# Performance work log

Measured on AMD Instinct MI355X. Metric: run time of the kernel, lower is better.

Reference implementation:

```python
import jax, jax.numpy as jnp
import numpy as np

EPS = 1e-5
NEG_SLOPE = 0.2

def _bn(x, gamma, beta):
    # BatchNorm1d in training mode: stats over (batch, length) per channel. x: [B,C,N]
    m = jnp.mean(x, axis=(0, 2), keepdims=True)
    v = jnp.mean((x - m) ** 2, axis=(0, 2), keepdims=True)  # biased variance
    return (x - m) * jax.lax.rsqrt(v + EPS) * gamma[None, :, None] + beta[None, :, None]

def setup_inputs() -> dict:
    key = jax.random.key(0)
    ks = jax.random.split(key, 7)
    B, C, N, H = 32, 64, 2048, 128
    s = 1.0 / np.sqrt(C)
    return {
        "x": jax.random.normal(ks[0], (B, C, N), dtype=jnp.float32),
        "wq": jax.random.normal(ks[1], (C, C), dtype=jnp.float32) * s,
        "wk": jax.random.normal(ks[2], (C, C), dtype=jnp.float32) * s,
        "wv": jax.random.normal(ks[3], (C, C), dtype=jnp.float32) * s,
        "w_ff1": jax.random.normal(ks[4], (H, C), dtype=jnp.float32) * s,
        "w_ff2": jax.random.normal(ks[5], (C, H), dtype=jnp.float32) * (1.0 / np.sqrt(H)),
        "bn1_gamma": jnp.ones((C,), dtype=jnp.float32),
        "bn1_beta": jnp.zeros((C,), dtype=jnp.float32),
        "bn2_gamma": jnp.ones((C,), dtype=jnp.float32),
        "bn2_beta": jnp.zeros((C,), dtype=jnp.float32),
    }

def reference(x, wq, wk, wv, w_ff1, w_ff2, bn1_gamma, bn1_beta, bn2_gamma, bn2_beta):
    # x: [B, C, N]; 1x1 convs are per-point channel matmuls
    C = x.shape[1]
    q = jnp.einsum('oc,bcn->bno', wq, x)          # [B,N,C]
    k = jnp.einsum('oc,bcn->bon', wk, x)          # [B,C,N]
    v = jnp.einsum('oc,bcn->bno', wv, x)          # [B,N,C] (v^T)
    energy = jnp.einsum('bnc,bcm->bnm', q, k)     # [B,N,N]
    attention = jax.nn.softmax(energy / jnp.sqrt(jnp.float32(C)), axis=-1)
    x_r = jnp.einsum('bnm,bmc->bcn', attention, v)  # [B,C,N]
    h = _bn(x + x_r, bn1_gamma, bn1_beta)
    ff = jnp.einsum('hc,bcn->bhn', w_ff1, h)      # [B,H,N]
    ff = jnp.where(ff >= 0, ff, NEG_SLOPE * ff)   # LeakyReLU(0.2)
    ff = jnp.einsum('ch,bhn->bcn', w_ff2, ff)     # [B,C,N]
    return _bn(h + ff, bn2_gamma, bn2_beta)
```

## Files before the change

### kernel.cpp

```cpp
#include <hip/hip_runtime.h>

#define B_ 32
#define C_ 64
#define N_ 2048
#define H_ 128

typedef unsigned short u16;
typedef unsigned int u32;
typedef float f32x4 __attribute__((ext_vector_type(4)));
typedef __bf16 bf16x8 __attribute__((ext_vector_type(8)));
typedef __bf16 bf16x4 __attribute__((ext_vector_type(4)));
typedef unsigned short u16x4 __attribute__((ext_vector_type(4)));

#define MFMA(a, b, c) __builtin_amdgcn_mfma_f32_16x16x32_bf16(a, b, c, 0, 0, 0)
#define LOG2E 1.44269504088896f

__device__ __forceinline__ int swz(int row, int cb) { return row * 128 + (cb ^ ((row & 7) << 4)); }
__device__ __forceinline__ int swz256(int row, int cb) { return row * 256 + (cb ^ ((row & 7) << 4)); }

__device__ __forceinline__ bf16x8 cvt8(const float* p, float s) {
    f32x4 a = *(const f32x4*)p, b = *(const f32x4*)(p + 4);
    bf16x8 o;
    o[0] = (__bf16)(a[0] * s); o[1] = (__bf16)(a[1] * s);
    o[2] = (__bf16)(a[2] * s); o[3] = (__bf16)(a[3] * s);
    o[4] = (__bf16)(b[0] * s); o[5] = (__bf16)(b[1] * s);
    o[6] = (__bf16)(b[2] * s); o[7] = (__bf16)(b[3] * s);
    return o;
}

__global__ __launch_bounds__(256) void qkv_k(
    const float* __restrict__ x,
    const float* __restrict__ wq, const float* __restrict__ wk, const float* __restrict__ wv,
    const float* __restrict__ w1, const float* __restrict__ w2,
    u16* __restrict__ Qg, u16* __restrict__ Kg, u16* __restrict__ Vg,
    u16* __restrict__ w1b, u16* __restrict__ w2b)
{
    const int b = blockIdx.y, nt = blockIdx.x, t = threadIdx.x;
    const int lane = t & 63, wave = t >> 6, g = lane >> 4, r16 = lane & 15;
    __shared__ __align__(16) u16 xT[128 * 64];
    const int n0 = nt * 128;

    bf16x8 wqf[4][2], wkf[4][2], wvf[4][2];
#pragma unroll
    for (int jt = 0; jt < 4; ++jt)
#pragma unroll
        for (int kc = 0; kc < 2; ++kc) {
            const int ro = (r16 + 16 * jt) * 64 + 8 * g + 32 * kc;
            wqf[jt][kc] = cvt8(wq + ro, 0.125f * LOG2E);
            wkf[jt][kc] = cvt8(wk + ro, 1.0f);
            wvf[jt][kc] = cvt8(wv + ro, 1.0f);
        }

    {
        int c = t >> 5;
        const int nn = (t & 31) * 4;
#pragma unroll
        for (int pass = 0; pass < 8; ++pass, c += 8) {
            f32x4 v = *(const f32x4*)&x[(size_t)(b * 64 + c) * 2048 + n0 + nn];
#pragma unroll
            for (int j = 0; j < 4; ++j)
                xT[swz(nn + j, 2 * c) >> 1] = __builtin_bit_cast(u16, (__bf16)v[j]);
        }
    }
    if (b == 0 && nt == 0) {
        for (int i = t; i < H_ * C_; i += 256) w1b[i] = __builtin_bit_cast(u16, (__bf16)w1[i]);
        for (int i = t; i < C_ * H_; i += 256) w2b[i] = __builtin_bit_cast(u16, (__bf16)w2[i]);
    }
    __syncthreads();

#pragma unroll
    for (int p = 0; p < 2; ++p) {
        const int nt16 = wave * 2 + p;
        bf16x8 xa[2];
#pragma unroll
        for (int kc = 0; kc < 2; ++kc)
            xa[kc] = *(const bf16x8*)&xT[swz(nt16 * 16 + r16, 16 * g + 64 * kc) >> 1];
#pragma unroll
        for (int jt = 0; jt < 4; ++jt) {
            f32x4 aq = {0.f, 0.f, 0.f, 0.f}, ak = {0.f, 0.f, 0.f, 0.f};
            aq = MFMA(wqf[jt][0], xa[0], aq); aq = MFMA(wqf[jt][1], xa[1], aq);
            ak = MFMA(wkf[jt][0], xa[0], ak); ak = MFMA(wkf[jt][1], xa[1], ak);
            bf16x4 qk, kk;
#pragma unroll
            for (int r = 0; r < 4; ++r) { qk[r] = (__bf16)aq[r]; kk[r] = (__bf16)ak[r]; }
            const size_t ro = (size_t)(b * 2048 + n0 + nt16 * 16 + r16) * 64 + 16 * jt + 4 * g;
            *(bf16x4*)&Qg[ro] = qk;
            *(bf16x4*)&Kg[ro] = kk;
        }
#pragma unroll
        for (int it = 0; it < 4; ++it) {
            f32x4 av = {0.f, 0.f, 0.f, 0.f};
            av = MFMA(xa[0], wvf[it][0], av);
            av = MFMA(xa[1], wvf[it][1], av);
            bf16x4 vk;
#pragma unroll
            for (int r = 0; r < 4; ++r) vk[r] = (__bf16)av[r];
            *(bf16x4*)&Vg[(size_t)(b * 64 + 16 * it + r16) * 2048 + n0 + nt16 * 16 + 4 * g] = vk;
        }
    }
}

__global__ __launch_bounds__(256) void attn_k(
    const u16* __restrict__ Qg, const u16* __restrict__ Kg, const u16* __restrict__ Vg,
    const float* __restrict__ x, float* __restrict__ y,
    float* __restrict__ ps, float* __restrict__ pq)
{
    const int t = threadIdx.x;
    const int lane = t & 63, wave = t >> 6, g = lane >> 4, r16 = lane & 15;
    const int L = blockIdx.x;
    const int xcd = L & 7, slot = L >> 3;
    const int b = xcd * 4 + (slot >> 4);
    const int qt = slot & 15;

    __shared__ __align__(16) u16 Kt[2][64 * 64];
    __shared__ __align__(16) u16 Vt[2][64 * 64];
    __shared__ __align__(16) u16 Pl[4][2][16 * 64];

    const int n0 = qt * 128 + wave * 32;
    bf16x8 qf[2][2];
#pragma unroll
    for (int u = 0; u < 2; ++u) {
        const u16* qrow = Qg + (size_t)(b * 2048 + n0 + 16 * u + r16) * 64 + 8 * g;
        qf[u][0] = *(const bf16x8*)qrow;
        qf[u][1] = *(const bf16x8*)(qrow + 32);
    }
    f32x4 xr[2][4];
#pragma unroll
    for (int u = 0; u < 2; ++u)
#pragma unroll
        for (int ct = 0; ct < 4; ++ct)
#pragma unroll
            for (int r = 0; r < 4; ++r)
                xr[u][ct][r] = x[(size_t)(b * 64 + 16 * ct + 4 * g + r) * 2048 + n0 + 16 * u + r16];

    f32x4 acc[2][4];
    float m[2] = {-1e30f, -1e30f}, lp[2] = {0.f, 0.f};
#pragma unroll
    for (int u = 0; u < 2; ++u)
#pragma unroll
        for (int ct = 0; ct < 4; ++ct) acc[u][ct] = (f32x4){0.f, 0.f, 0.f, 0.f};

    const char* Kgb = (const char*)Kg + (size_t)b * 2048 * 128;
    const char* Vgb = (const char*)Vg + (size_t)b * 64 * 4096;
    const int srcxor = (((lane & 7) ^ (lane >> 3)) << 4);
    const int rowb = wave * 16 + (lane >> 3);

    auto stage = [&](int kv, int buf) {
#pragma unroll
        for (int j = 0; j < 2; ++j) {
            const char* gk = Kgb + (size_t)(kv + rowb + 8 * j) * 128 + srcxor;
            const char* gv = Vgb + (size_t)(rowb + 8 * j) * 4096 + kv * 2 + srcxor;
            char* lk = (char*)&Kt[buf][0] + (wave * 2 + j) * 1024;
            char* lv = (char*)&Vt[buf][0] + (wave * 2 + j) * 1024;
            __builtin_amdgcn_global_load_lds(
                (const __attribute__((address_space(1))) void*)gk,
                (__attribute__((address_space(3))) void*)lk, 16, 0, 0);
            __builtin_amdgcn_global_load_lds(
                (const __attribute__((address_space(1))) void*)gv,
                (__attribute__((address_space(3))) void*)lv, 16, 0, 0);
        }
    };

    stage(0, 0);

#pragma unroll 1
    for (int kvt = 0; kvt < 32; ++kvt) {
        __syncthreads();
        if (kvt < 31) stage((kvt + 1) * 64, (kvt + 1) & 1);
        const char* Kc = (const char*)&Kt[kvt & 1][0];
        const char* Vc = (const char*)&Vt[kvt & 1][0];

        bf16x8 kf[4][2];
#pragma unroll
        for (int it = 0; it < 4; ++it)
#pragma unroll
            for (int kc = 0; kc < 2; ++kc)
                kf[it][kc] = *(const bf16x8*)(Kc + swz(16 * it + r16, 16 * g + 64 * kc));
        f32x4 s[2][4];
#pragma unroll
        for (int it = 0; it < 4; ++it) {
            f32x4 a0 = {0.f, 0.f, 0.f, 0.f}, a1 = {0.f, 0.f, 0.f, 0.f};
            a0 = MFMA(kf[it][0], qf[0][0], a0); a0 = MFMA(kf[it][1], qf[0][1], a0);
            a1 = MFMA(kf[it][0], qf[1][0], a1); a1 = MFMA(kf[it][1], qf[1][1], a1);
            s[0][it] = a0; s[1][it] = a1;
        }
        bf16x8 vf[4][2];
#pragma unroll
        for (int ct = 0; ct < 4; ++ct)
#pragma unroll
            for (int kc = 0; kc < 2; ++kc)
                vf[ct][kc] = *(const bf16x8*)(Vc + swz(16 * ct + r16, 16 * g + 64 * kc));

#pragma unroll
        for (int u = 0; u < 2; ++u) {
            float pm = s[u][0][0];
#pragma unroll
            for (int it = 0; it < 4; ++it)
#pragma unroll
                for (int r = 0; r < 4; ++r) pm = fmaxf(pm, s[u][it][r]);
            pm = fmaxf(pm, __shfl_xor(pm, 16, 64));
            pm = fmaxf(pm, __shfl_xor(pm, 32, 64));
            if (!__all(pm <= m[u] + 8.f)) {
                const float mn = fmaxf(m[u], pm);
                const float al = exp2f(m[u] - mn);
                m[u] = mn;
                lp[u] *= al;
#pragma unroll
                for (int ct = 0; ct < 4; ++ct)
#pragma unroll
                    for (int r = 0; r < 4; ++r) acc[u][ct][r] *= al;
            }
            float ls = 0.f;
#pragma unroll
            for (int it = 0; it < 4; ++it) {
                bf16x4 pk;
#pragma unroll
                for (int r = 0; r < 4; ++r) {
                    const float pv = exp2f(s[u][it][r] - m[u]);
                    ls += pv;
                    pk[r] = (__bf16)pv;
                }
                *(bf16x4*)((char*)Pl[wave][u] + swz(r16, 32 * it + 8 * g)) = pk;
            }
            lp[u] += ls;
            const bf16x8 pf0 = *(const bf16x8*)((const char*)Pl[wave][u] + swz(r16, 16 * g));
            const bf16x8 pf1 = *(const bf16x8*)((const char*)Pl[wave][u] + swz(r16, 16 * g + 64));
#pragma unroll
            for (int ct = 0; ct < 4; ++ct) {
                acc[u][ct] = MFMA(vf[ct][0], pf0, acc[u][ct]);
                acc[u][ct] = MFMA(vf[ct][1], pf1, acc[u][ct]);
            }
        }
    }

    float sv[4][4], qv[4][4];
#pragma unroll
    for (int ct = 0; ct < 4; ++ct)
#pragma unroll
        for (int r = 0; r < 4; ++r) { sv[ct][r] = 0.f; qv[ct][r] = 0.f; }
#pragma unroll
    for (int u = 0; u < 2; ++u) {
        float l = lp[u];
        l += __shfl_xor(l, 16, 64);
        l += __shfl_xor(l, 32, 64);
        const float inv = 1.0f / l;
        const int n = n0 + 16 * u + r16;
#pragma unroll
        for (int ct = 0; ct < 4; ++ct) {
            f32x4 o;
#pragma unroll
            for (int r = 0; r < 4; ++r) {
                o[r] = acc[u][ct][r] * inv + xr[u][ct][r];
                sv[ct][r] += o[r];
                qv[ct][r] += o[r] * o[r];
            }
            *(f32x4*)&y[(size_t)(b * 2048 + n) * 64 + 16 * ct + 4 * g] = o;
        }
    }
#pragma unroll
    for (int d = 1; d <= 8; d <<= 1)
#pragma unroll
        for (int ct = 0; ct < 4; ++ct)
#pragma unroll
            for (int r = 0; r < 4; ++r) {
                sv[ct][r] += __shfl_xor(sv[ct][r], d, 64);
                qv[ct][r] += __shfl_xor(qv[ct][r], d, 64);
            }
    __syncthreads();
    float* sb = (float*)&Pl[0][0][0];
    if (r16 == 0) {
#pragma unroll
        for (int ct = 0; ct < 4; ++ct)
#pragma unroll
            for (int r = 0; r < 4; ++r) {
                const int c = 16 * ct + 4 * g + r;
                sb[wave * 64 + c] = sv[ct][r];
                sb[256 + wave * 64 + c] = qv[ct][r];
            }
    }
    __syncthreads();
    if (t < 64) {
        ps[L * 64 + t] = sb[t] + sb[64 + t] + sb[128 + t] + sb[192 + t];
        pq[L * 64 + t] = sb[256 + t] + sb[320 + t] + sb[384 + t] + sb[448 + t];
    }
}

__global__ __launch_bounds__(256) void finalize_k(
    const float* __restrict__ psum, const float* __restrict__ psq,
    const float* __restrict__ gamma, const float* __restrict__ beta,
    float* __restrict__ ss, int nblk)
{
    const int c = blockIdx.x, t = threadIdx.x;
    const int lane = t & 63, wave = t >> 6;
    float s = 0.f, q = 0.f;
    for (int bl = t; bl < nblk; bl += 256) {
        s += psum[bl * 64 + c];
        q += psq[bl * 64 + c];
    }
#pragma unroll
    for (int d = 1; d <= 32; d <<= 1) {
        s += __shfl_xor(s, d, 64);
        q += __shfl_xor(q, d, 64);
    }
    __shared__ float ls[4], lq[4];
    if (lane == 0) { ls[wave] = s; lq[wave] = q; }
    __syncthreads();
    if (t == 0) {
        s = ls[0] + ls[1] + ls[2] + ls[3];
        q = lq[0] + lq[1] + lq[2] + lq[3];
        const float mean = s * (1.0f / 65536.0f);
        const float var  = q * (1.0f / 65536.0f) - mean * mean;
        const float sc   = rsqrtf(var + 1e-5f) * gamma[c];
        ss[c] = sc;
        ss[64 + c] = beta[c] - mean * sc;
    }
}

__global__ __launch_bounds__(256) void ff_k(
    const float* __restrict__ y, const float* __restrict__ ss1,
    const u16* __restrict__ w1b, const u16* __restrict__ w2b,
    float* __restrict__ z, float* __restrict__ ps, float* __restrict__ pq)
{
    const int b = blockIdx.y, nt = blockIdx.x, t = threadIdx.x;
    const int lane = t & 63, wave = t >> 6, g = lane >> 4, r16 = lane & 15;
    const int L = blockIdx.y * gridDim.x + blockIdx.x;
    __shared__ __align__(16) u16 hT[64 * 64];
    __shared__ __align__(16) float hf[64 * 68];
    __shared__ __align__(16) u16 pb[4][16 * 128];
    __shared__ float sc1[64], sh1[64];
    if (t < 64) { sc1[t] = ss1[t]; sh1[t] = ss1[64 + t]; }
    __syncthreads();
    const int n0 = nt * 64;
    {
        const int i = t >> 2, c0 = (t & 3) * 16;
        u16 hb[16] __attribute__((aligned(16)));
#pragma unroll
        for (int q4 = 0; q4 < 4; ++q4) {
            const int c = c0 + 4 * q4;
            f32x4 v = *(const f32x4*)&y[(size_t)(b * 2048 + n0 + i) * 64 + c];
            f32x4 hv;
#pragma unroll
            for (int j = 0; j < 4; ++j) hv[j] = v[j] * sc1[c + j] + sh1[c + j];
            *(f32x4*)&hf[i * 68 + c] = hv;
#pragma unroll
            for (int j = 0; j < 4; ++j) hb[4 * q4 + j] = __builtin_bit_cast(u16, (__bf16)hv[j]);
        }
        *(uint4*)&hT[swz(i, 2 * c0) >> 1]      = *(const uint4*)&hb[0];
        *(uint4*)&hT[swz(i, 2 * c0 + 16) >> 1] = *(const uint4*)&hb[8];
    }
    __syncthreads();

    bf16x8 ha[2];
#pragma unroll
    for (int kc = 0; kc < 2; ++kc)
        ha[kc] = *(const bf16x8*)&hT[swz(wave * 16 + r16, 16 * g + 64 * kc) >> 1];
#pragma unroll
    for (int it = 0; it < 8; ++it) {
        f32x4 a = {0.f, 0.f, 0.f, 0.f};
#pragma unroll
        for (int kc = 0; kc < 2; ++kc) {
            bf16x8 w1f = *(const bf16x8*)&w1b[(r16 + 16 * it) * 64 + 8 * g + 32 * kc];
            a = MFMA(w1f, ha[kc], a);
        }
        u16x4 pk;
#pragma unroll
        for (int r = 0; r < 4; ++r) {
            const float rv = a[r] >= 0.f ? a[r] : 0.2f * a[r];
            pk[r] = __builtin_bit_cast(u16, (__bf16)rv);
        }
        *(u16x4*)&pb[wave][swz256(r16, 2 * (16 * it + 4 * g)) >> 1] = pk;
    }
    bf16x8 pa[4];
#pragma unroll
    for (int kc = 0; kc < 4; ++kc)
        pa[kc] = *(const bf16x8*)&pb[wave][swz256(r16, 16 * g + 64 * kc) >> 1];
    const int nl = wave * 16 + r16;
    float sv[4][4], qv[4][4];
#pragma unroll
    for (int jt = 0; jt < 4; ++jt) {
        f32x4 a = {0.f, 0.f, 0.f, 0.f};
#pragma unroll
        for (int kc = 0; kc < 4; ++kc) {
            bf16x8 w2f = *(const bf16x8*)&w2b[(r16 + 16 * jt) * 128 + 8 * g + 32 * kc];
            a = MFMA(w2f, pa[kc], a);
        }
        f32x4 h4 = *(const f32x4*)&hf[nl * 68 + 16 * jt + 4 * g];
#pragma unroll
        for (int r = 0; r < 4; ++r) {
            a[r] += h4[r];
            sv[jt][r] = a[r];
            qv[jt][r] = a[r] * a[r];
        }
        *(f32x4*)&z[(size_t)(b * 2048 + n0 + nl) * 64 + 16 * jt + 4 * g] = a;
    }
#pragma unroll
    for (int d = 1; d <= 8; d <<= 1)
#pragma unroll
        for (int jt = 0; jt < 4; ++jt)
#pragma unroll
            for (int r = 0; r < 4; ++r) {
                sv[jt][r] += __shfl_xor(sv[jt][r], d, 64);
                qv[jt][r] += __shfl_xor(qv[jt][r], d, 64);
            }
    __syncthreads();
    float* sb = (float*)&pb[0][0];
    if (r16 == 0) {
#pragma unroll
        for (int jt = 0; jt < 4; ++jt)
#pragma unroll
            for (int r = 0; r < 4; ++r) {
                const int c = 16 * jt + 4 * g + r;
                sb[wave * 64 + c] = sv[jt][r];
                sb[256 + wave * 64 + c] = qv[jt][r];
            }
    }
    __syncthreads();
    if (t < 64) {
        ps[L * 64 + t] = sb[t] + sb[64 + t] + sb[128 + t] + sb[192 + t];
        pq[L * 64 + t] = sb[256 + t] + sb[320 + t] + sb[384 + t] + sb[448 + t];
    }
}

__global__ __launch_bounds__(256) void bnout_k(
    const float* __restrict__ z, const float* __restrict__ ss2, float* __restrict__ out)
{
    const int b = blockIdx.y, nt = blockIdx.x, t = threadIdx.x;
    __shared__ float tile[64 * 65];
    __shared__ float sc2[64], sh2[64];
    if (t < 64) { sc2[t] = ss2[t]; sh2[t] = ss2[64 + t]; }
    __syncthreads();
    const int n0 = nt * 64;
    {
        const int i = t >> 2, c0 = (t & 3) * 16;
#pragma unroll
        for (int q4 = 0; q4 < 4; ++q4) {
            const int c = c0 + 4 * q4;
            f32x4 v = *(const f32x4*)&z[(size_t)(b * 2048 + n0 + i) * 64 + c];
#pragma unroll
            for (int j = 0; j < 4; ++j)
                tile[(i)*65 + c + j] = v[j] * sc2[c + j] + sh2[c + j];
        }
    }
    __syncthreads();
    {
        const int c = t >> 2, j0 = (t & 3) * 16;
#pragma unroll
        for (int q4 = 0; q4 < 4; ++q4) {
            f32x4 ov;
#pragma unroll
            for (int j = 0; j < 4; ++j)
                ov[j] = tile[(j0 + 4 * q4 + j) * 65 + c];
            *(f32x4*)&out[(size_t)(b * 64 + c) * 2048 + n0 + j0 + 4 * q4] = ov;
        }
    }
}

extern "C" void kernel_launch(void* const* d_in, const int* in_sizes, int n_in,
                              void* d_out, int out_size, void* d_ws, size_t ws_size,
                              hipStream_t stream)
{
    const float* x   = (const float*)d_in[0];
    const float* wq  = (const float*)d_in[1];
    const float* wk  = (const float*)d_in[2];
    const float* wv  = (const float*)d_in[3];
    const float* w1  = (const float*)d_in[4];
    const float* w2  = (const float*)d_in[5];
    const float* g1  = (const float*)d_in[6];
    const float* be1 = (const float*)d_in[7];
    const float* g2  = (const float*)d_in[8];
    const float* be2 = (const float*)d_in[9];
    float* out = (float*)d_out;

    char* w = (char*)d_ws;
    u16* Qg = (u16*)w;   w += (size_t)B_ * N_ * C_ * 2;
    u16* Kg = (u16*)w;   w += (size_t)B_ * N_ * C_ * 2;
    u16* Vg = (u16*)w;   w += (size_t)B_ * N_ * C_ * 2;
    float* y = (float*)w; w += (size_t)B_ * N_ * C_ * 4;
    float* z = (float*)w; w += (size_t)B_ * N_ * C_ * 4;
    u16* w1b = (u16*)w;  w += (size_t)H_ * C_ * 2;
    u16* w2b = (u16*)w;  w += (size_t)C_ * H_ * 2;
    float* ps1 = (float*)w; w += 1024 * 64 * 4;
    float* pq1 = (float*)w; w += 1024 * 64 * 4;
    float* ps2 = (float*)w; w += 1024 * 64 * 4;
    float* pq2 = (float*)w; w += 1024 * 64 * 4;
    float* ss1 = (float*)w; w += 128 * 4;
    float* ss2 = (float*)w; w += 128 * 4;

    const dim3 blk(256);
    hipLaunchKernelGGL(qkv_k,   dim3(16, 32), blk, 0, stream, x, wq, wk, wv, w1, w2, Qg, Kg, Vg, w1b, w2b);
    hipLaunchKernelGGL(attn_k,  dim3(512),    blk, 0, stream, Qg, Kg, Vg, x, y, ps1, pq1);
    hipLaunchKernelGGL(finalize_k, dim3(64),  blk, 0, stream, ps1, pq1, g1, be1, ss1, 512);
    hipLaunchKernelGGL(ff_k,    dim3(32, 32), blk, 0, stream, y, ss1, w1b, w2b, z, ps2, pq2);
    hipLaunchKernelGGL(finalize_k, dim3(64),  blk, 0, stream, ps2, pq2, g2, be2, ss2, 1024);
    hipLaunchKernelGGL(bnout_k, dim3(32, 32), blk, 0, stream, z, ss2, out);
}
```

Baseline: 152.9 us.

## Store intermediates y and z in bf16 and restructure attention loop with setprio

The fp32 intermediates y and z become bf16, halving the traffic written by attn_k and ff_k and read back by ff_k and bnout_k. The attention kernel now uses one flat LDS buffer with precomputed swizzled offsets and manual double-buffer unrolling. It adds s_setprio around the MFMA blocks and tree-structured max and sum reductions. The residual x is loaded at the epilogue instead of being held in registers across the loop. The change adds bf16 rounding error to the residual stream before each BatchNorm.

```diff
diff --git a/kernel.cpp b/kernel.cpp
--- a/kernel.cpp
+++ b/kernel.cpp
@@ -17,6 +17,10 @@
 
 __device__ __forceinline__ int swz(int row, int cb) { return row * 128 + (cb ^ ((row & 7) << 4)); }
 __device__ __forceinline__ int swz256(int row, int cb) { return row * 256 + (cb ^ ((row & 7) << 4)); }
+
+__device__ __forceinline__ float b2f(u16 v) {
+    union { u32 u; float f; } x; x.u = ((u32)v) << 16; return x.f;
+}
 
 __device__ __forceinline__ bf16x8 cvt8(const float* p, float s) {
     f32x4 a = *(const f32x4*)p, b = *(const f32x4*)(p + 4);
@@ -102,7 +106,7 @@
 
 __global__ __launch_bounds__(256) void attn_k(
     const u16* __restrict__ Qg, const u16* __restrict__ Kg, const u16* __restrict__ Vg,
-    const float* __restrict__ x, float* __restrict__ y,
+    const float* __restrict__ x, u16* __restrict__ yb,
     float* __restrict__ ps, float* __restrict__ pq)
 {
     const int t = threadIdx.x;
@@ -112,9 +116,8 @@
     const int b = xcd * 4 + (slot >> 4);
     const int qt = slot & 15;
 
-    __shared__ __align__(16) u16 Kt[2][64 * 64];
-    __shared__ __align__(16) u16 Vt[2][64 * 64];
-    __shared__ __align__(16) u16 Pl[4][2][16 * 64];
+    __shared__ __align__(16) u16 Lds16[24576];
+    char* lds = (char*)Lds16;
 
     const int n0 = qt * 128 + wave * 32;
     bf16x8 qf[2][2];
@@ -124,14 +127,6 @@
         qf[u][0] = *(const bf16x8*)qrow;
         qf[u][1] = *(const bf16x8*)(qrow + 32);
     }
-    f32x4 xr[2][4];
-#pragma unroll
-    for (int u = 0; u < 2; ++u)
-#pragma unroll
-        for (int ct = 0; ct < 4; ++ct)
-#pragma unroll
-            for (int r = 0; r < 4; ++r)
-                xr[u][ct][r] = x[(size_t)(b * 64 + 16 * ct + 4 * g + r) * 2048 + n0 + 16 * u + r16];
 
     f32x4 acc[2][4];
     float m[2] = {-1e30f, -1e30f}, lp[2] = {0.f, 0.f};
@@ -145,92 +140,114 @@
     const int srcxor = (((lane & 7) ^ (lane >> 3)) << 4);
     const int rowb = wave * 16 + (lane >> 3);
 
-    auto stage = [&](int kv, int buf) {
+    int ka[8];
+#pragma unroll
+    for (int i = 0; i < 8; ++i)
+        ka[i] = swz(16 * (i >> 1) + r16, 16 * g + 64 * (i & 1));
+    const int pbase = 32768 + wave * 4096;
+    int pw[2][4], pr[2][2];
+#pragma unroll
+    for (int u = 0; u < 2; ++u) {
+#pragma unroll
+        for (int it = 0; it < 4; ++it) pw[u][it] = pbase + u * 2048 + swz(r16, 32 * it + 8 * g);
+#pragma unroll
+        for (int kc = 0; kc < 2; ++kc) pr[u][kc] = pbase + u * 2048 + swz(r16, 16 * g + 64 * kc);
+    }
+
+    auto stage = [&](int kvt, int buf) {
 #pragma unroll
         for (int j = 0; j < 2; ++j) {
-            const char* gk = Kgb + (size_t)(kv + rowb + 8 * j) * 128 + srcxor;
-            const char* gv = Vgb + (size_t)(rowb + 8 * j) * 4096 + kv * 2 + srcxor;
-            char* lk = (char*)&Kt[buf][0] + (wave * 2 + j) * 1024;
-            char* lv = (char*)&Vt[buf][0] + (wave * 2 + j) * 1024;
+            const char* gk = Kgb + (size_t)(kvt * 64 + rowb + 8 * j) * 128 + srcxor;
+            const char* gv = Vgb + (size_t)(rowb + 8 * j) * 4096 + kvt * 128 + srcxor;
+            char* lk = lds + buf * 8192 + (wave * 2 + j) * 1024;
             __builtin_amdgcn_global_load_lds(
                 (const __attribute__((address_space(1))) void*)gk,
                 (__attribute__((address_space(3))) void*)lk, 16, 0, 0);
             __builtin_amdgcn_global_load_lds(
                 (const __attribute__((address_space(1))) void*)gv,
-                (__attribute__((address_space(3))) void*)lv, 16, 0, 0);
+                (__attribute__((address_space(3))) void*)(lk + 16384), 16, 0, 0);
         }
     };
 
-    stage(0, 0);
-
-#pragma unroll 1
-    for (int kvt = 0; kvt < 32; ++kvt) {
+    auto tile = [&](int kvt, int buf) {
         __syncthreads();
-        if (kvt < 31) stage((kvt + 1) * 64, (kvt + 1) & 1);
-        const char* Kc = (const char*)&Kt[kvt & 1][0];
-        const char* Vc = (const char*)&Vt[kvt & 1][0];
-
-        bf16x8 kf[4][2];
-#pragma unroll
-        for (int it = 0; it < 4; ++it)
-#pragma unroll
-            for (int kc = 0; kc < 2; ++kc)
-                kf[it][kc] = *(const bf16x8*)(Kc + swz(16 * it + r16, 16 * g + 64 * kc));
+        if (kvt + 1 < 32) stage(kvt + 1, buf ^ 1);
+        const char* Kc = lds + buf * 8192;
+        const char* Vc = Kc + 16384;
+
+        bf16x8 kf[8];
+#pragma unroll
+        for (int i = 0; i < 8; ++i) kf[i] = *(const bf16x8*)(Kc + ka[i]);
         f32x4 s[2][4];
+        __builtin_amdgcn_s_setprio(1);
 #pragma unroll
         for (int it = 0; it < 4; ++it) {
             f32x4 a0 = {0.f, 0.f, 0.f, 0.f}, a1 = {0.f, 0.f, 0.f, 0.f};
-            a0 = MFMA(kf[it][0], qf[0][0], a0); a0 = MFMA(kf[it][1], qf[0][1], a0);
-            a1 = MFMA(kf[it][0], qf[1][0], a1); a1 = MFMA(kf[it][1], qf[1][1], a1);
+            a0 = MFMA(kf[2 * it], qf[0][0], a0); a0 = MFMA(kf[2 * it + 1], qf[0][1], a0);
+            a1 = MFMA(kf[2 * it], qf[1][0], a1); a1 = MFMA(kf[2 * it + 1], qf[1][1], a1);
             s[0][it] = a0; s[1][it] = a1;
         }
-        bf16x8 vf[4][2];
-#pragma unroll
-        for (int ct = 0; ct < 4; ++ct)
-#pragma unroll
-            for (int kc = 0; kc < 2; ++kc)
-                vf[ct][kc] = *(const bf16x8*)(Vc + swz(16 * ct + r16, 16 * g + 64 * kc));
+        __builtin_amdgcn_s_setprio(0);
+        bf16x8 vf[8];
+#pragma unroll
+        for (int i = 0; i < 8; ++i) vf[i] = *(const bf16x8*)(Vc + ka[i]);
 
 #pragma unroll
         for (int u = 0; u < 2; ++u) {
-            float pm = s[u][0][0];
+            float mi[4];
 #pragma unroll
             for (int it = 0; it < 4; ++it)
-#pragma unroll
-                for (int r = 0; r < 4; ++r) pm = fmaxf(pm, s[u][it][r]);
+                mi[it] = fmaxf(fmaxf(s[u][it][0], s[u][it][1]),
+                               fmaxf(s[u][it][2], s[u][it][3]));
+            float pm = fmaxf(fmaxf(mi[0], mi[1]), fmaxf(mi[2], mi[3]));
             pm = fmaxf(pm, __shfl_xor(pm, 16, 64));
             pm = fmaxf(pm, __shfl_xor(pm, 32, 64));
             if (!__all(pm <= m[u] + 8.f)) {
                 const float mn = fmaxf(m[u], pm);
                 const float al = exp2f(m[u] - mn);
-                m[u] = mn;
-                lp[u] *= al;
+                m[u] = mn; lp[u] *= al;
 #pragma unroll
                 for (int ct = 0; ct < 4; ++ct)
 #pragma unroll
                     for (int r = 0; r < 4; ++r) acc[u][ct][r] *= al;
             }
-            float ls = 0.f;
+            float ts[4];
 #pragma unroll
             for (int it = 0; it < 4; ++it) {
+                const float p0 = exp2f(s[u][it][0] - m[u]);
+                const float p1 = exp2f(s[u][it][1] - m[u]);
+                const float p2 = exp2f(s[u][it][2] - m[u]);
+                const float p3 = exp2f(s[u][it][3] - m[u]);
+                ts[it] = (p0 + p1) + (p2 + p3);
                 bf16x4 pk;
-#pragma unroll
-                for (int r = 0; r < 4; ++r) {
-                    const float pv = exp2f(s[u][it][r] - m[u]);
-                    ls += pv;
-                    pk[r] = (__bf16)pv;
-                }
-                *(bf16x4*)((char*)Pl[wave][u] + swz(r16, 32 * it + 8 * g)) = pk;
-            }
-            lp[u] += ls;
-            const bf16x8 pf0 = *(const bf16x8*)((const char*)Pl[wave][u] + swz(r16, 16 * g));
-            const bf16x8 pf1 = *(const bf16x8*)((const char*)Pl[wave][u] + swz(r16, 16 * g + 64));
+                pk[0] = (__bf16)p0; pk[1] = (__bf16)p1;
+                pk[2] = (__bf16)p2; pk[3] = (__bf16)p3;
+                *(bf16x4*)(lds + pw[u][it]) = pk;
+            }
+            lp[u] += (ts[0] + ts[1]) + (ts[2] + ts[3]);
+        }
+        bf16x8 pf[2][2];
+#pragma unroll
+        for (int u = 0; u < 2; ++u) {
+            pf[u][0] = *(const bf16x8*)(lds + pr[u][0]);
+            pf[u][1] = *(const bf16x8*)(lds + pr[u][1]);
+        }
+        __builtin_amdgcn_s_setprio(1);
+#pragma unroll
+        for (int u = 0; u < 2; ++u)
 #pragma unroll
             for (int ct = 0; ct < 4; ++ct) {
-                acc[u][ct] = MFMA(vf[ct][0], pf0, acc[u][ct]);
-                acc[u][ct] = MFMA(vf[ct][1], pf1, acc[u][ct]);
-            }
-        }
+                acc[u][ct] = MFMA(vf[2 * ct], pf[u][0], acc[u][ct]);
+                acc[u][ct] = MFMA(vf[2 * ct + 1], pf[u][1], acc[u][ct]);
+            }
+        __builtin_amdgcn_s_setprio(0);
+    };
+
+    stage(0, 0);
+#pragma unroll 1
+    for (int kvt = 0; kvt < 32; kvt += 2) {
+        tile(kvt, 0);
+        tile(kvt + 1, 1);
     }
 
     float sv[4][4], qv[4][4];
@@ -247,14 +264,16 @@
         const int n = n0 + 16 * u + r16;
 #pragma unroll
         for (int ct = 0; ct < 4; ++ct) {
-            f32x4 o;
+            bf16x4 ov;
 #pragma unroll
             for (int r = 0; r < 4; ++r) {
-                o[r] = acc[u][ct][r] * inv + xr[u][ct][r];
-                sv[ct][r] += o[r];
-                qv[ct][r] += o[r] * o[r];
-            }
-            *(f32x4*)&y[(size_t)(b * 2048 + n) * 64 + 16 * ct + 4 * g] = o;
+                const int c = 16 * ct + 4 * g + r;
+                const float o = acc[u][ct][r] * inv + x[(size_t)(b * 64 + c) * 2048 + n];
+                sv[ct][r] += o;
+                qv[ct][r] += o * o;
+                ov[r] = (__bf16)o;
+            }
+            *(bf16x4*)&yb[(size_t)(b * 2048 + n) * 64 + 16 * ct + 4 * g] = ov;
         }
     }
 #pragma unroll
@@ -267,7 +286,7 @@
                 qv[ct][r] += __shfl_xor(qv[ct][r], d, 64);
             }
     __syncthreads();
-    float* sb = (float*)&Pl[0][0][0];
+    float* sb = (float*)(lds + 32768);
     if (r16 == 0) {
 #pragma unroll
         for (int ct = 0; ct < 4; ++ct)
@@ -317,9 +336,9 @@
 }
 
 __global__ __launch_bounds__(256) void ff_k(
-    const float* __restrict__ y, const float* __restrict__ ss1,
+    const u16* __restrict__ y, const float* __restrict__ ss1,
     const u16* __restrict__ w1b, const u16* __restrict__ w2b,
-    float* __restrict__ z, float* __restrict__ ps, float* __restrict__ pq)
+    u16* __restrict__ zb, float* __restrict__ ps, float* __restrict__ pq)
 {
     const int b = blockIdx.y, nt = blockIdx.x, t = threadIdx.x;
     const int lane = t & 63, wave = t >> 6, g = lane >> 4, r16 = lane & 15;
@@ -333,17 +352,16 @@
     const int n0 = nt * 64;
     {
         const int i = t >> 2, c0 = (t & 3) * 16;
+        u16 yb16[16] __attribute__((aligned(16)));
+        *(uint4*)&yb16[0] = *(const uint4*)&y[(size_t)(b * 2048 + n0 + i) * 64 + c0];
+        *(uint4*)&yb16[8] = *(const uint4*)&y[(size_t)(b * 2048 + n0 + i) * 64 + c0 + 8];
         u16 hb[16] __attribute__((aligned(16)));
 #pragma unroll
-        for (int q4 = 0; q4 < 4; ++q4) {
-            const int c = c0 + 4 * q4;
-            f32x4 v = *(const f32x4*)&y[(size_t)(b * 2048 + n0 + i) * 64 + c];
-            f32x4 hv;
-#pragma unroll
-            for (int j = 0; j < 4; ++j) hv[j] = v[j] * sc1[c + j] + sh1[c + j];
-            *(f32x4*)&hf[i * 68 + c] = hv;
-#pragma unroll
-            for (int j = 0; j < 4; ++j) hb[4 * q4 + j] = __builtin_bit_cast(u16, (__bf16)hv[j]);
+        for (int j = 0; j < 16; ++j) {
+            const int c = c0 + j;
+            const float hv = b2f(yb16[j]) * sc1[c] + sh1[c];
+            hf[i * 68 + c] = hv;
+            hb[j] = __builtin_bit_cast(u16, (__bf16)hv);
         }
         *(uint4*)&hT[swz(i, 2 * c0) >> 1]      = *(const uint4*)&hb[0];
         *(uint4*)&hT[swz(i, 2 * c0 + 16) >> 1] = *(const uint4*)&hb[8];
@@ -385,13 +403,15 @@
             a = MFMA(w2f, pa[kc], a);
         }
         f32x4 h4 = *(const f32x4*)&hf[nl * 68 + 16 * jt + 4 * g];
+        bf16x4 zk;
 #pragma unroll
         for (int r = 0; r < 4; ++r) {
             a[r] += h4[r];
             sv[jt][r] = a[r];
             qv[jt][r] = a[r] * a[r];
-        }
-        *(f32x4*)&z[(size_t)(b * 2048 + n0 + nl) * 64 + 16 * jt + 4 * g] = a;
+            zk[r] = (__bf16)a[r];
+        }
+        *(bf16x4*)&zb[(size_t)(b * 2048 + n0 + nl) * 64 + 16 * jt + 4 * g] = zk;
     }
 #pragma unroll
     for (int d = 1; d <= 8; d <<= 1)
@@ -422,7 +442,7 @@
 }
 
 __global__ __launch_bounds__(256) void bnout_k(
-    const float* __restrict__ z, const float* __restrict__ ss2, float* __restrict__ out)
+    const u16* __restrict__ zb, const float* __restrict__ ss2, float* __restrict__ out)
 {
     const int b = blockIdx.y, nt = blockIdx.x, t = threadIdx.x;
     __shared__ float tile[64 * 65];
@@ -432,13 +452,13 @@
     const int n0 = nt * 64;
     {
         const int i = t >> 2, c0 = (t & 3) * 16;
-#pragma unroll
-        for (int q4 = 0; q4 < 4; ++q4) {
-            const int c = c0 + 4 * q4;
-            f32x4 v = *(const f32x4*)&z[(size_t)(b * 2048 + n0 + i) * 64 + c];
-#pragma unroll
-            for (int j = 0; j < 4; ++j)
-                tile[(i)*65 + c + j] = v[j] * sc2[c + j] + sh2[c + j];
+        u16 zb16[16] __attribute__((aligned(16)));
+        *(uint4*)&zb16[0] = *(const uint4*)&zb[(size_t)(b * 2048 + n0 + i) * 64 + c0];
+        *(uint4*)&zb16[8] = *(const uint4*)&zb[(size_t)(b * 2048 + n0 + i) * 64 + c0 + 8];
+#pragma unroll
+        for (int j = 0; j < 16; ++j) {
+            const int c = c0 + j;
+            tile[i * 65 + c] = b2f(zb16[j]) * sc2[c] + sh2[c];
         }
     }
     __syncthreads();
@@ -475,8 +495,8 @@
     u16* Qg = (u16*)w;   w += (size_t)B_ * N_ * C_ * 2;
     u16* Kg = (u16*)w;   w += (size_t)B_ * N_ * C_ * 2;
     u16* Vg = (u16*)w;   w += (size_t)B_ * N_ * C_ * 2;
-    float* y = (float*)w; w += (size_t)B_ * N_ * C_ * 4;
-    float* z = (float*)w; w += (size_t)B_ * N_ * C_ * 4;
+    u16* yb = (u16*)w;   w += (size_t)B_ * N_ * C_ * 2;
+    u16* zb = (u16*)w;   w += (size_t)B_ * N_ * C_ * 2;
     u16* w1b = (u16*)w;  w += (size_t)H_ * C_ * 2;
     u16* w2b = (u16*)w;  w += (size_t)C_ * H_ * 2;
     float* ps1 = (float*)w; w += 1024 * 64 * 4;
@@ -488,9 +508,9 @@
 
     const dim3 blk(256);
     hipLaunchKernelGGL(qkv_k,   dim3(16, 32), blk, 0, stream, x, wq, wk, wv, w1, w2, Qg, Kg, Vg, w1b, w2b);
-    hipLaunchKernelGGL(attn_k,  dim3(512),    blk, 0, stream, Qg, Kg, Vg, x, y, ps1, pq1);
+    hipLaunchKernelGGL(attn_k,  dim3(512),    blk, 0, stream, Qg, Kg, Vg, x, yb, ps1, pq1);
     hipLaunchKernelGGL(finalize_k, dim3(64),  blk, 0, stream, ps1, pq1, g1, be1, ss1, 512);
-    hipLaunchKernelGGL(ff_k,    dim3(32, 32), blk, 0, stream, y, ss1, w1b, w2b, z, ps2, pq2);
+    hipLaunchKernelGGL(ff_k,    dim3(32, 32), blk, 0, stream, yb, ss1, w1b, w2b, zb, ps2, pq2);
     hipLaunchKernelGGL(finalize_k, dim3(64),  blk, 0, stream, ps2, pq2, g2, be2, ss2, 1024);
-    hipLaunchKernelGGL(bnout_k, dim3(32, 32), blk, 0, stream, z, ss2, out);
-}
+    hipLaunchKernelGGL(bnout_k, dim3(32, 32), blk, 0, stream, zb, ss2, out);
+}
```

Result: faster. 144.9 us (-5.3%).
